# Optimization experiments

Hardware: AMD Instinct MI355X
Metric: run time of the kernel (lower is better)

Reference implementation:

```python
import jax, jax.numpy as jnp
import numpy as np

B, D, H, W = 4, 64, 64, 64
S = 64          # number of attention segments
N = 8192        # query pixels
K = 4           # n_refs
HID = 256
D9 = D * 9      # feat_unfold 3x3
IN_DIM = D9 + 2 + 2  # +rel_coord +rel_cell


def setup_inputs() -> dict:
    key = jax.random.key(0)
    ks = jax.random.split(key, 10)
    feat = jax.random.normal(ks[0], (B, D, H, W), jnp.float32)
    attn_sftmx = jax.nn.softmax(jax.random.normal(ks[1], (B, H * W, S), jnp.float32), axis=2)
    coord = jax.random.uniform(ks[2], (B, N, 2), jnp.float32) * 2.0 - 1.0  # [-1,1]
    cell = jnp.full((B, N, 2), 2.0 / 256.0, jnp.float32)  # HR cell size for 256x256 output
    def lin(k, fi, fo):
        return jax.random.normal(k, (fi, fo), jnp.float32) / np.sqrt(fi).astype(np.float32)
    w0 = lin(ks[3], IN_DIM, HID); b0 = jnp.zeros((HID,), jnp.float32)
    w1 = lin(ks[4], HID, HID);    b1 = jnp.zeros((HID,), jnp.float32)
    w2 = lin(ks[5], HID, HID);    b2 = jnp.zeros((HID,), jnp.float32)
    w3 = lin(ks[6], HID, HID);    b3 = jnp.zeros((HID,), jnp.float32)
    w4 = lin(ks[7], HID, 3);      b4 = jnp.zeros((3,), jnp.float32)
    return dict(feat=feat, attn_sftmx=attn_sftmx, coord=coord, cell=cell,
                w0=w0, b0=b0, w1=w1, b1=b1, w2=w2, b2=b2, w3=w3, b3=b3, w4=w4, b4=b4)


def _imnet(x, w0, b0, w1, b1, w2, b2, w3, b3, w4, b4):
    h = jax.nn.relu(x @ w0 + b0)
    h = jax.nn.relu(h @ w1 + b1)
    h = jax.nn.relu(h @ w2 + b2)
    h = jax.nn.relu(h @ w3 + b3)
    return h @ w4 + b4


def reference(feat, attn_sftmx, coord, cell, w0, b0, w1, b1, w2, b2, w3, b3, w4, b4):
    Bn, Dc, h, w = feat.shape
    Nq = coord.shape[1]
    hw = h * w
    # ---- feat_unfold: F.unfold(feat, 3, padding=1) -> (B, D*9, h, w), channel order c*9 + ki*3 + kj
    pad = jnp.pad(feat, ((0, 0), (0, 0), (1, 1), (1, 1)))
    patches = jnp.stack([pad[:, :, ki:ki + h, kj:kj + w]
                         for ki in range(3) for kj in range(3)], axis=2)  # (B,D,9,h,w)
    d9 = Dc * 9
    feat_rows = patches.reshape(Bn, d9, h, w).transpose(0, 2, 3, 1).reshape(Bn, hw, d9)  # (B,hw,D9)
    scale_hw = jnp.array([h, w], jnp.float32)
    rel_cell = cell * scale_hw  # (B,N,2)

    # ================= attention ensemble =================
    pc = (coord + 1.0) / 2.0 * scale_hw
    pc = jnp.clip(pc.astype(jnp.int32), 0, hw - 1)
    pc1d = pc[..., 0] * h + pc[..., 1]  # (B,N)
    segm_idx_whole = jnp.argmax(attn_sftmx, axis=2)  # (B,hw)
    segm_idx = jnp.take_along_axis(segm_idx_whole, pc1d, axis=1)  # (B,N)
    attn_t = attn_sftmx.transpose(0, 2, 1)  # (B,S,hw)
    prob_map = jnp.take_along_axis(attn_t, segm_idx[:, :, None], axis=1)  # (B,N,hw)
    ref_probs, ref_coords = jax.lax.top_k(prob_map, K)  # (B,N,K)
    # Faithful to original: ref_coords (values in [0,hw)) index the FLATTENED (B*hw, D9)
    # feature table, i.e. all batches gather batch-0 rows (source-code behavior).
    ref_feats = feat_rows.reshape(Bn * hw, d9)[ref_coords]  # (B,N,K,D9)
    rrc = ref_coords - pc1d[..., None]  # (B,N,K) int
    rel0 = jnp.floor_divide(rrc, h).astype(jnp.float32) / h
    rel1 = jnp.mod(rrc, h).astype(jnp.float32) / w
    rel = jnp.stack([rel0, rel1], axis=-1)  # (B,N,K,2)
    rc_b = jnp.broadcast_to(rel_cell[:, :, None, :], (Bn, Nq, K, 2))
    inp_attn = jnp.concatenate([ref_feats, rel, rc_b], axis=-1)  # (B,N,K,IN)
    pred_attn = _imnet(inp_attn.reshape(-1, inp_attn.shape[-1]),
                       w0, b0, w1, b1, w2, b2, w3, b3, w4, b4).reshape(Bn, Nq, K, -1)
    wprob = ref_probs / jnp.sum(ref_probs, axis=-1, keepdims=True)
    ret_attn = jnp.sum(pred_attn * wprob[..., None], axis=2)  # (B,N,3)

    # ================= local ensemble =================
    rx, ry = 1.0 / h, 1.0 / w  # 2/h/2, 2/w/2
    eps = 1e-6
    offs = jnp.array([[-1., -1.], [-1., 1.], [1., -1.], [1., 1.]], jnp.float32) \
           * jnp.array([rx, ry], jnp.float32) + eps  # (4,2)
    c = jnp.clip(coord[None] + offs[:, None, None, :], -1 + 1e-6, 1 - 1e-6)  # (4,B,N,2)
    # grid_sample nearest, align_corners=False (grid flipped -> c[...,0] is height)
    iy = jnp.clip(jnp.rint(((c[..., 0] + 1.0) * h - 1.0) / 2.0), 0, h - 1).astype(jnp.int32)
    ix = jnp.clip(jnp.rint(((c[..., 1] + 1.0) * w - 1.0) / 2.0), 0, w - 1).astype(jnp.int32)
    flat = iy * w + ix  # (4,B,N)
    bidx = jnp.arange(Bn)[None, :, None]
    q_feat = feat_rows[bidx, flat]  # (4,B,N,D9)
    qc0 = -1.0 + (2.0 * iy.astype(jnp.float32) + 1.0) / h  # make_coord centers
    qc1 = -1.0 + (2.0 * ix.astype(jnp.float32) + 1.0) / w
    rel_coord = jnp.stack([(coord[None, ..., 0] - qc0) * h,
                           (coord[None, ..., 1] - qc1) * w], axis=-1)  # (4,B,N,2)
    rc_l = jnp.broadcast_to(rel_cell[None], (4, Bn, Nq, 2))
    inp_loc = jnp.concatenate([q_feat, rel_coord, rc_l], axis=-1)  # (4,B,N,IN)
    pred_loc = _imnet(inp_loc.reshape(-1, inp_loc.shape[-1]),
                      w0, b0, w1, b1, w2, b2, w3, b3, w4, b4).reshape(4, Bn, Nq, -1)
    area = jnp.abs(rel_coord[..., 0] * rel_coord[..., 1]) + 1e-9  # (4,B,N)
    tot = jnp.sum(area, axis=0)
    wts = area[::-1] / tot[None]  # area swap 0<->3, 1<->2 == reverse
    ret_local = jnp.sum(pred_loc * wts[..., None], axis=0)  # (B,N,3)

    total = float(K + 4)
    return ret_attn * (K / total) + ret_local * (4.0 / total)
```

## Files before the change

### kernel.cpp

```cpp
#include <hip/hip_runtime.h>
#include <hip/hip_bf16.h>
#include <math.h>
#include <stdint.h>

#define B_ 4
#define D_ 64
#define H_ 64
#define W_ 64
#define S_ 64
#define N_ 8192
#define K_ 4
#define HID_ 256
#define HW_ 4096
#define NQ_ (B_*N_)
#define ROWS_ (NQ_*8)

typedef _Float16 h8   __attribute__((ext_vector_type(8)));
typedef _Float16 h4   __attribute__((ext_vector_type(4)));
typedef float    f32x4 __attribute__((ext_vector_type(4)));

__global__ void fused_prep_kernel(const float* __restrict__ feat,
                                  const float* __restrict__ attn,
                                  const float* __restrict__ w0,
                                  const float* __restrict__ w1,
                                  const float* __restrict__ w2,
                                  const float* __restrict__ w3,
                                  const float* __restrict__ w4,
                                  _Float16* __restrict__ featT,
                                  float* __restrict__ attnT,
                                  _Float16* __restrict__ w0F,
                                  _Float16* __restrict__ wF123,
                                  float* __restrict__ w4T,
                                  float* __restrict__ w0tail,
                                  int* __restrict__ segm)
{
  __shared__ float t[64][65];
  int blk = blockIdx.x;
  int tid = threadIdx.x;

  if (blk < 256) {
    int b = blk >> 6, y = blk & 63;
    for (int p = 0; p < 16; ++p) {
      int c = p * 4 + (tid >> 6), x = tid & 63;
      t[c][x] = feat[(((size_t)b * 64 + c) << 12) + (y << 6) + x];
    }
    __syncthreads();
    for (int p = 0; p < 16; ++p) {
      int x = p * 4 + (tid >> 6), c = tid & 63;
      featT[((((size_t)b * 64 + y) * 64 + x) << 6) + c] = (_Float16)t[c][x];
    }
    return;
  }
  blk -= 256;
  if (blk < 256) {
    int b = blk >> 6, j0 = (blk & 63) << 6;
    for (int idx = tid; idx < 4096; idx += 256) {
      int r = idx >> 6, c = idx & 63;
      t[r][c] = attn[((size_t)(b * 4096 + j0 + r)) * 64 + c];
    }
    __syncthreads();
    for (int idx = tid; idx < 4096; idx += 256) {
      int s = idx >> 6, r = idx & 63;
      attnT[((size_t)(b * 64 + s)) * 4096 + j0 + r] = t[r][s];
    }
    return;
  }
  blk -= 256;
  if (blk < 1351) {
    int i = blk * 256 + tid;
    if (i < 147456) {
      int g = i / 36864, rem = i - g * 36864;
      int ks = rem >> 11, rem2 = rem & 2047;
      int cb = rem2 >> 9, e = rem2 & 511;
      int lane = e >> 3, j = e & 7;
      int n = g * 64 + cb * 16 + (lane & 15);
      int k = ks * 32 + (lane >> 4) * 8 + j;
      int kk = k >> 6, cc = k & 63;
      w0F[i] = (_Float16)w0[(cc * 9 + kk) * 256 + n];
      return;
    }
    i -= 147456;
    if (i < 196608) {
      int l = i >> 16, rem = i & 65535;
      int g = rem >> 14, rem2 = rem & 16383;
      int ks = rem2 >> 11, rem3 = rem2 & 2047;
      int cb = rem3 >> 9, e = rem3 & 511;
      int lane = e >> 3, j = e & 7;
      int n = g * 64 + cb * 16 + (lane & 15);
      int k = ks * 32 + (lane >> 4) * 8 + j;
      const float* w = (l == 0) ? w1 : (l == 1) ? w2 : w3;
      wF123[i] = (_Float16)w[k * 256 + n];
      return;
    }
    i -= 196608;
    if (i < 768) { int j = i / 256, c = i - j * 256; w4T[i] = w4[c * 3 + j]; return; }
    i -= 768;
    if (i < 1024) { int j = i >> 8, n = i & 255; w0tail[i] = w0[(576 + j) * 256 + n]; }
    return;
  }
  blk -= 1351;
  {
    int p = blk * 256 + tid;
    if (p >= B_ * HW_) return;
    const float* a = attn + (size_t)p * S_;
    float best = a[0]; int bi = 0;
    for (int s = 1; s < S_; ++s) { float v = a[s]; if (v > best) { best = v; bi = s; } }
    segm[p] = bi;
  }
}

__global__ void topk_kernel(const float* __restrict__ attnT,
                            int* __restrict__ refc, float* __restrict__ wprob)
{
  int bid = blockIdx.x;
  int tid = threadIdx.x;
  __shared__ float sv[256]; __shared__ int si[256];
  __shared__ float cvs[4]; __shared__ int cis[4];

  const float* col = attnT + (size_t)bid * 4096;
  float tv[4] = { -INFINITY, -INFINITY, -INFINITY, -INFINITY };
  int   ti[4] = { 0x7fffffff, 0x7fffffff, 0x7fffffff, 0x7fffffff };
  for (int j = tid; j < HW_; j += 256) {
    float v = col[j];
    if (v > tv[3]) {
      tv[3] = v; ti[3] = j;
      #pragma unroll
      for (int x = 3; x > 0; --x) {
        if (tv[x] > tv[x-1] || (tv[x] == tv[x-1] && ti[x] < ti[x-1])) {
          float fv = tv[x]; tv[x] = tv[x-1]; tv[x-1] = fv;
          int   fi = ti[x]; ti[x] = ti[x-1]; ti[x-1] = fi;
        }
      }
    }
  }
  int ptr = 0;
  for (int r = 0; r < 4; ++r) {
    sv[tid] = (ptr < 4) ? tv[ptr] : -INFINITY;
    si[tid] = (ptr < 4) ? ti[ptr] : 0x7fffffff;
    __syncthreads();
    for (int o = 128; o; o >>= 1) {
      if (tid < o) {
        float v2 = sv[tid + o]; int i2 = si[tid + o];
        if (v2 > sv[tid] || (v2 == sv[tid] && i2 < si[tid])) { sv[tid] = v2; si[tid] = i2; }
      }
      __syncthreads();
    }
    if (tid == 0) { cvs[r] = sv[0]; cis[r] = si[0]; }
    __syncthreads();
    if (ptr < 4 && ti[ptr] == cis[r]) ptr++;
    __syncthreads();
  }
  if (tid == 0) {
    float ssum = cvs[0] + cvs[1] + cvs[2] + cvs[3];
    for (int k = 0; k < 4; ++k) { refc[bid*4 + k] = cis[k]; wprob[bid*4 + k] = cvs[k] / ssum; }
  }
}

__global__ void meta_kernel(const float* __restrict__ coord, const float* __restrict__ cell,
                            const int* __restrict__ segm, const int* __restrict__ refc,
                            const float* __restrict__ wprob,
                            int* __restrict__ msrc, float4* __restrict__ mt,
                            float* __restrict__ mwgt)
{
  int q = blockIdx.x * 256 + threadIdx.x;
  if (q >= NQ_) return;
  int b = q >> 13;
  float c0 = coord[2*q], c1 = coord[2*q + 1];
  float rc0 = cell[2*q] * 64.0f, rc1 = cell[2*q + 1] * 64.0f;

  float pf0 = (c0 + 1.0f) / 2.0f * 64.0f;
  float pf1 = (c1 + 1.0f) / 2.0f * 64.0f;
  int pc0 = (int)pf0, pc1 = (int)pf1;
  pc0 = min(max(pc0, 0), 4095); pc1 = min(max(pc1, 0), 4095);
  int pc1d = pc0 * 64 + pc1;
  int sg = segm[b * 4096 + min(pc1d, 4095)];
  int base = (b * 64 + sg) * 4;
  #pragma unroll
  for (int k = 0; k < 4; ++k) {
    int rc = refc[base + k];
    int rrc = rc - pc1d;
    float rel0 = (float)(rrc >> 6) * 0.015625f;
    float rel1 = (float)(rrc & 63) * 0.015625f;
    int r = q * 8 + k;
    msrc[r] = rc;
    mt[r] = make_float4(rel0, rel1, rc0, rc1);
    mwgt[r] = 0.5f * wprob[base + k];
  }

  const float sg0[4] = { -1.f, -1.f, 1.f, 1.f };
  const float sg1[4] = { -1.f,  1.f, -1.f, 1.f };
  float area[4], rr0[4], rr1[4]; int srcs[4];
  #pragma unroll
  for (int t = 0; t < 4; ++t) {
    float o0 = sg0[t] * 0.015625f + 1e-6f;
    float o1 = sg1[t] * 0.015625f + 1e-6f;
    float cc0 = fminf(fmaxf(c0 + o0, -1.0f + 1e-6f), 1.0f - 1e-6f);
    float cc1 = fminf(fmaxf(c1 + o1, -1.0f + 1e-6f), 1.0f - 1e-6f);
    float vy = ((cc0 + 1.0f) * 64.0f - 1.0f) / 2.0f;
    float vx = ((cc1 + 1.0f) * 64.0f - 1.0f) / 2.0f;
    float fy = fminf(fmaxf(rintf(vy), 0.0f), 63.0f);
    float fx = fminf(fmaxf(rintf(vx), 0.0f), 63.0f);
    int iy = (int)fy, ix = (int)fx;
    srcs[t] = b * 4096 + iy * 64 + ix;
    float qc0 = -1.0f + (2.0f * (float)iy + 1.0f) / 64.0f;
    float qc1 = -1.0f + (2.0f * (float)ix + 1.0f) / 64.0f;
    float r0 = (c0 - qc0) * 64.0f;
    float r1 = (c1 - qc1) * 64.0f;
    rr0[t] = r0; rr1[t] = r1;
    area[t] = fabsf(r0 * r1) + 1e-9f;
  }
  float tot = area[0] + area[1] + area[2] + area[3];
  #pragma unroll
  for (int t = 0; t < 4; ++t) {
    int r = q * 8 + 4 + t;
    msrc[r] = srcs[t];
    mt[r] = make_float4(rr0[t], rr1[t], rc0, rc1);
    mwgt[r] = 0.5f * area[3 - t] / tot;
  }
}

__launch_bounds__(256, 4)
__global__ void p0_kernel(const _Float16* __restrict__ featT,
                          const _Float16* __restrict__ w0F,
                          float* __restrict__ P0)
{
  int blk = blockIdx.x;
  int b = blk >> 8, y = (blk >> 2) & 63, qr = blk & 3;
  int tid = threadIdx.x;
  int wave = tid >> 6, lane = tid & 63, quad = lane >> 4, l16 = lane & 15;

  f32x4 acc[4];
  #pragma unroll
  for (int j = 0; j < 4; j++) { f32x4 z = {0.f,0.f,0.f,0.f}; acc[j] = z; }
  h8 zero8 = {0,0,0,0,0,0,0,0};

  #pragma unroll
  for (int ks = 0; ks < 18; ++ks) {
    int k0 = ks * 32 + quad * 8;
    int kk = k0 >> 6, cc = k0 & 63;
    int di = kk / 3 - 1, dj = kk - (kk / 3) * 3 - 1;
    int yy = y + di;
    int xx = qr * 16 + l16 + dj;
    h8 afr;
    if ((unsigned)yy < 64u && (unsigned)xx < 64u)
      afr = *(const h8*)(featT + ((((size_t)b * 64 + yy) * 64 + xx) << 6) + cc);
    else
      afr = zero8;
    #pragma unroll
    for (int cb = 0; cb < 4; cb++) {
      h8 bfr = *(const h8*)(w0F + ((((size_t)wave * 18 + ks) * 4 + cb) << 9) + lane * 8);
      acc[cb] = __builtin_amdgcn_mfma_f32_16x16x32_f16(afr, bfr, acc[cb], 0, 0, 0);
    }
  }
  int pixbase = (b * 4096 + y * 64 + qr * 16);
  #pragma unroll
  for (int cb = 0; cb < 4; cb++)
    #pragma unroll
    for (int i = 0; i < 4; i++) {
      int m = quad * 4 + i;
      int n = wave * 64 + cb * 16 + l16;
      P0[((size_t)(pixbase + m) << 8) + n] = acc[cb][i];
    }
}

__launch_bounds__(256, 2)
__global__ void trunk_kernel(const float* __restrict__ P0,
                             const int* __restrict__ msrc,
                             const float4* __restrict__ mt,
                             const float* __restrict__ mwgt,
                             const float* __restrict__ w0tail,
                             const float* __restrict__ b0,
                             const _Float16* __restrict__ wF123,
                             const float* __restrict__ b1,
                             const float* __restrict__ b2,
                             const float* __restrict__ b3,
                             const float* __restrict__ w4T,
                             const float* __restrict__ b4,
                             float* __restrict__ out)
{
  __shared__ _Float16 hS[128][264];
  __shared__ float part_s[128][2][3];
  __shared__ float red[128][4];

  int tid = threadIdx.x;
  int rowbase = blockIdx.x * 128;
  int wv = tid >> 6;

  {
    int cg = tid & 63;
    float4 wt0 = ((const float4*)w0tail)[cg];
    float4 wt1 = ((const float4*)w0tail)[64 + cg];
    float4 wt2 = ((const float4*)w0tail)[128 + cg];
    float4 wt3 = ((const float4*)w0tail)[192 + cg];
    float4 bb  = ((const float4*)b0)[cg];
    #pragma unroll 1
    for (int g = 0; g < 4; ++g) {
      int srcs[8]; float4 ts[8];
      #pragma unroll
      for (int i = 0; i < 8; ++i) {
        int r = rowbase + g * 32 + i * 4 + wv;
        srcs[i] = msrc[r];
        ts[i] = mt[r];
      }
      #pragma unroll
      for (int i = 0; i < 8; ++i) {
        int rr = g * 32 + i * 4 + wv;
        float4 t = ts[i];
        float4 p = ((const float4*)(P0 + ((size_t)srcs[i] << 8)))[cg];
        h4 v;
        v[0] = (_Float16)fmaxf(p.x + t.x*wt0.x + t.y*wt1.x + t.z*wt2.x + t.w*wt3.x + bb.x, 0.0f);
        v[1] = (_Float16)fmaxf(p.y + t.x*wt0.y + t.y*wt1.y + t.z*wt2.y + t.w*wt3.y + bb.y, 0.0f);
        v[2] = (_Float16)fmaxf(p.z + t.x*wt0.z + t.y*wt1.z + t.z*wt2.z + t.w*wt3.z + bb.z, 0.0f);
        v[3] = (_Float16)fmaxf(p.w + t.x*wt0.w + t.y*wt1.w + t.z*wt2.w + t.w*wt3.w + bb.w, 0.0f);
        *(h4*)(&hS[rr][cg * 4]) = v;
      }
    }
  }
  __syncthreads();

  int wave = tid >> 6, lane = tid & 63, quad = lane >> 4, l16 = lane & 15;

  #pragma unroll 1
  for (int l = 0; l < 3; ++l) {
    const _Float16* wL = wF123 + (((size_t)l * 4 + wave) << 14);
    const float* bia = (l == 0) ? b1 : (l == 1) ? b2 : b3;
    f32x4 acc[8][4];
    #pragma unroll
    for (int i = 0; i < 8; i++)
      #pragma unroll
      for (int j = 0; j < 4; j++) { f32x4 z = {0.f,0.f,0.f,0.f}; acc[i][j] = z; }

    h8 bP[2][4];
    #pragma unroll
    for (int cb = 0; cb < 4; cb++) {
      bP[0][cb] = *(const h8*)(wL + (((size_t)0 * 4 + cb) << 9) + lane * 8);
      bP[1][cb] = *(const h8*)(wL + (((size_t)1 * 4 + cb) << 9) + lane * 8);
    }

    #pragma unroll
    for (int ks = 0; ks < 8; ++ks) {
      int cur = ks & 1;
      int k0 = ks * 32 + quad * 8;
      h8 afr[8];
      #pragma unroll
      for (int rb = 0; rb < 8; rb++)
        afr[rb] = *(const h8*)(&hS[rb * 16 + l16][k0]);
      #pragma unroll
      for (int rb = 0; rb < 8; rb++)
        #pragma unroll
        for (int cb = 0; cb < 4; cb++)
          acc[rb][cb] = __builtin_amdgcn_mfma_f32_16x16x32_f16(afr[rb], bP[cur][cb], acc[rb][cb], 0, 0, 0);
      if (ks + 2 < 8) {
        #pragma unroll
        for (int cb = 0; cb < 4; cb++)
          bP[cur][cb] = *(const h8*)(wL + (((size_t)(ks + 2) * 4 + cb) << 9) + lane * 8);
      }
    }
    __syncthreads();
    #pragma unroll
    for (int rb = 0; rb < 8; rb++)
      #pragma unroll
      for (int cb = 0; cb < 4; cb++) {
        int n = wave * 64 + cb * 16 + l16;
        float bv = bia[n];
        #pragma unroll
        for (int i = 0; i < 4; i++) {
          int m = rb * 16 + quad * 4 + i;
          hS[m][n] = (_Float16)fmaxf(acc[rb][cb][i] + bv, 0.0f);
        }
      }
    __syncthreads();
  }

  {
    int row = tid >> 1, part = tid & 1;
    const _Float16* hr = &hS[row][part * 128];
    float s0 = 0.f, s1 = 0.f, s2 = 0.f;
    #pragma unroll
    for (int c8 = 0; c8 < 128; c8 += 8) {
      h8 hv = *(const h8*)(hr + c8);
      #pragma unroll
      for (int u = 0; u < 8; ++u) {
        float h = (float)hv[u];
        int c = part * 128 + c8 + u;
        s0 += h * w4T[c];
        s1 += h * w4T[256 + c];
        s2 += h * w4T[512 + c];
      }
    }
    part_s[row][part][0] = s0; part_s[row][part][1] = s1; part_s[row][part][2] = s2;
  }
  __syncthreads();
  if (tid < 128) {
    float wgt = mwgt[rowbase + tid];
    red[tid][0] = (part_s[tid][0][0] + part_s[tid][1][0] + b4[0]) * wgt;
    red[tid][1] = (part_s[tid][0][1] + part_s[tid][1][1] + b4[1]) * wgt;
    red[tid][2] = (part_s[tid][0][2] + part_s[tid][1][2] + b4[2]) * wgt;
  }
  __syncthreads();
  if (tid < 16) {
    int q = blockIdx.x * 16 + tid;
    float o0 = 0.f, o1 = 0.f, o2 = 0.f;
    #pragma unroll
    for (int j = 0; j < 8; j++) {
      o0 += red[tid * 8 + j][0];
      o1 += red[tid * 8 + j][1];
      o2 += red[tid * 8 + j][2];
    }
    out[q * 3 + 0] = o0;
    out[q * 3 + 1] = o1;
    out[q * 3 + 2] = o2;
  }
}

extern "C" void kernel_launch(void* const* d_in, const int* in_sizes, int n_in,
                              void* d_out, int out_size, void* d_ws, size_t ws_size,
                              hipStream_t stream)
{
  const float* feat  = (const float*)d_in[0];
  const float* attn  = (const float*)d_in[1];
  const float* coord = (const float*)d_in[2];
  const float* cell  = (const float*)d_in[3];
  const float* w0 = (const float*)d_in[4];
  const float* b0 = (const float*)d_in[5];
  const float* w1 = (const float*)d_in[6];
  const float* b1 = (const float*)d_in[7];
  const float* w2 = (const float*)d_in[8];
  const float* b2 = (const float*)d_in[9];
  const float* w3 = (const float*)d_in[10];
  const float* b3 = (const float*)d_in[11];
  const float* w4 = (const float*)d_in[12];
  const float* b4 = (const float*)d_in[13];
  float* out = (float*)d_out;

  char* ws = (char*)d_ws;
  size_t off = 0;
  auto alloc = [&](size_t bytes) -> char* {
    char* p = ws + off;
    off += (bytes + 255) & ~(size_t)255;
    return p;
  };
  _Float16* featT = (_Float16*)alloc((size_t)B_ * H_ * W_ * D_ * 2);
  _Float16* w0F   = (_Float16*)alloc((size_t)147456 * 2);
  _Float16* wF123 = (_Float16*)alloc((size_t)196608 * 2);
  float*  w4T   = (float*)alloc((size_t)3 * 256 * 4);
  float*  w0tl  = (float*)alloc((size_t)4 * 256 * 4);
  float*  attnT = (float*)alloc((size_t)B_ * S_ * HW_ * 4);
  int*    segm  = (int*)alloc((size_t)B_ * HW_ * 4);
  int*    refc  = (int*)alloc((size_t)B_ * S_ * K_ * 4);
  float*  wprob = (float*)alloc((size_t)B_ * S_ * K_ * 4);
  float*  P0    = (float*)alloc((size_t)B_ * HW_ * 256 * 4);
  int*    msrc  = (int*)alloc((size_t)ROWS_ * 4);
  float4* mtb   = (float4*)alloc((size_t)ROWS_ * 16);
  float*  mwgt  = (float*)alloc((size_t)ROWS_ * 4);
  (void)in_sizes; (void)n_in; (void)out_size; (void)ws_size;

  fused_prep_kernel<<<1927, 256, 0, stream>>>(feat, attn, w0, w1, w2, w3, w4,
                                              featT, attnT, w0F, wF123, w4T, w0tl, segm);
  topk_kernel<<<256, 256, 0, stream>>>(attnT, refc, wprob);
  meta_kernel<<<128, 256, 0, stream>>>(coord, cell, segm, refc, wprob, msrc, mtb, mwgt);
  p0_kernel<<<1024, 256, 0, stream>>>(featT, w0F, P0);
  trunk_kernel<<<2048, 256, 0, stream>>>(P0, msrc, mtb, mwgt, w0tl, b0, wF123,
                                         b1, b2, b3, w4T, b4, out);
}
```

Baseline: 302.2 us.

## Store P0 in fp16, widen p0 tiles, and reorder final linear reduction

The p0 kernel now computes a full 64-pixel row per block with 4x4 MFMA accumulators, so each block loads the weight fragments once instead of once per 16-pixel quarter. P0 is written as fp16 instead of fp32, which halves both the write traffic and the gathered reads in the trunk. The final layer now takes the weighted sum over each query's 8 rows before the 256x3 dot product, using linearity, and scales b4 by the summed weights. This cuts the last-layer multiply work by about 8x. The cost is lower occupancy in p0, fewer blocks in its grid, and extra fp16 rounding of the precomputed first-layer activations.

```diff
diff --git a/kernel.cpp b/kernel.cpp
--- a/kernel.cpp
+++ b/kernel.cpp
@@ -219,19 +219,21 @@
   }
 }
 
-__launch_bounds__(256, 4)
+__launch_bounds__(256, 2)
 __global__ void p0_kernel(const _Float16* __restrict__ featT,
                           const _Float16* __restrict__ w0F,
-                          float* __restrict__ P0)
+                          _Float16* __restrict__ P0h)
 {
   int blk = blockIdx.x;
-  int b = blk >> 8, y = (blk >> 2) & 63, qr = blk & 3;
+  int b = blk >> 6, y = blk & 63;
   int tid = threadIdx.x;
   int wave = tid >> 6, lane = tid & 63, quad = lane >> 4, l16 = lane & 15;
 
-  f32x4 acc[4];
-  #pragma unroll
-  for (int j = 0; j < 4; j++) { f32x4 z = {0.f,0.f,0.f,0.f}; acc[j] = z; }
+  f32x4 acc[4][4];
+  #pragma unroll
+  for (int i = 0; i < 4; i++)
+    #pragma unroll
+    for (int j = 0; j < 4; j++) { f32x4 z = {0.f,0.f,0.f,0.f}; acc[i][j] = z; }
   h8 zero8 = {0,0,0,0,0,0,0,0};
 
   #pragma unroll
@@ -240,31 +242,40 @@
     int kk = k0 >> 6, cc = k0 & 63;
     int di = kk / 3 - 1, dj = kk - (kk / 3) * 3 - 1;
     int yy = y + di;
-    int xx = qr * 16 + l16 + dj;
-    h8 afr;
-    if ((unsigned)yy < 64u && (unsigned)xx < 64u)
-      afr = *(const h8*)(featT + ((((size_t)b * 64 + yy) * 64 + xx) << 6) + cc);
-    else
-      afr = zero8;
-    #pragma unroll
-    for (int cb = 0; cb < 4; cb++) {
-      h8 bfr = *(const h8*)(w0F + ((((size_t)wave * 18 + ks) * 4 + cb) << 9) + lane * 8);
-      acc[cb] = __builtin_amdgcn_mfma_f32_16x16x32_f16(afr, bfr, acc[cb], 0, 0, 0);
-    }
-  }
-  int pixbase = (b * 4096 + y * 64 + qr * 16);
-  #pragma unroll
-  for (int cb = 0; cb < 4; cb++)
-    #pragma unroll
-    for (int i = 0; i < 4; i++) {
-      int m = quad * 4 + i;
-      int n = wave * 64 + cb * 16 + l16;
-      P0[((size_t)(pixbase + m) << 8) + n] = acc[cb][i];
-    }
+    h8 afr[4];
+    #pragma unroll
+    for (int rb = 0; rb < 4; rb++) {
+      int xx = rb * 16 + l16 + dj;
+      if ((unsigned)yy < 64u && (unsigned)xx < 64u)
+        afr[rb] = *(const h8*)(featT + ((((size_t)b * 64 + yy) * 64 + xx) << 6) + cc);
+      else
+        afr[rb] = zero8;
+    }
+    h8 bfr[4];
+    #pragma unroll
+    for (int cb = 0; cb < 4; cb++)
+      bfr[cb] = *(const h8*)(w0F + ((((size_t)wave * 18 + ks) * 4 + cb) << 9) + lane * 8);
+    #pragma unroll
+    for (int rb = 0; rb < 4; rb++)
+      #pragma unroll
+      for (int cb = 0; cb < 4; cb++)
+        acc[rb][cb] = __builtin_amdgcn_mfma_f32_16x16x32_f16(afr[rb], bfr[cb], acc[rb][cb], 0, 0, 0);
+  }
+  int pixbase = blk * 64;
+  #pragma unroll
+  for (int rb = 0; rb < 4; rb++)
+    #pragma unroll
+    for (int cb = 0; cb < 4; cb++)
+      #pragma unroll
+      for (int i = 0; i < 4; i++) {
+        int m = rb * 16 + quad * 4 + i;
+        int n = wave * 64 + cb * 16 + l16;
+        P0h[((size_t)(pixbase + m) << 8) + n] = (_Float16)acc[rb][cb][i];
+      }
 }
 
 __launch_bounds__(256, 2)
-__global__ void trunk_kernel(const float* __restrict__ P0,
+__global__ void trunk_kernel(const _Float16* __restrict__ P0h,
                              const int* __restrict__ msrc,
                              const float4* __restrict__ mt,
                              const float* __restrict__ mwgt,
@@ -279,12 +290,15 @@
                              float* __restrict__ out)
 {
   __shared__ _Float16 hS[128][264];
-  __shared__ float part_s[128][2][3];
-  __shared__ float red[128][4];
+  __shared__ float mwL[128];
+  __shared__ float swL[16];
+  __shared__ float partB[16][3][4];
 
   int tid = threadIdx.x;
   int rowbase = blockIdx.x * 128;
   int wv = tid >> 6;
+
+  if (tid < 128) mwL[tid] = mwgt[rowbase + tid];
 
   {
     int cg = tid & 63;
@@ -306,12 +320,12 @@
       for (int i = 0; i < 8; ++i) {
         int rr = g * 32 + i * 4 + wv;
         float4 t = ts[i];
-        float4 p = ((const float4*)(P0 + ((size_t)srcs[i] << 8)))[cg];
+        h4 pv = *(const h4*)(P0h + ((size_t)srcs[i] << 8) + cg * 4);
         h4 v;
-        v[0] = (_Float16)fmaxf(p.x + t.x*wt0.x + t.y*wt1.x + t.z*wt2.x + t.w*wt3.x + bb.x, 0.0f);
-        v[1] = (_Float16)fmaxf(p.y + t.x*wt0.y + t.y*wt1.y + t.z*wt2.y + t.w*wt3.y + bb.y, 0.0f);
-        v[2] = (_Float16)fmaxf(p.z + t.x*wt0.z + t.y*wt1.z + t.z*wt2.z + t.w*wt3.z + bb.z, 0.0f);
-        v[3] = (_Float16)fmaxf(p.w + t.x*wt0.w + t.y*wt1.w + t.z*wt2.w + t.w*wt3.w + bb.w, 0.0f);
+        v[0] = (_Float16)fmaxf((float)pv[0] + t.x*wt0.x + t.y*wt1.x + t.z*wt2.x + t.w*wt3.x + bb.x, 0.0f);
+        v[1] = (_Float16)fmaxf((float)pv[1] + t.x*wt0.y + t.y*wt1.y + t.z*wt2.y + t.w*wt3.y + bb.y, 0.0f);
+        v[2] = (_Float16)fmaxf((float)pv[2] + t.x*wt0.z + t.y*wt1.z + t.z*wt2.z + t.w*wt3.z + bb.z, 0.0f);
+        v[3] = (_Float16)fmaxf((float)pv[3] + t.x*wt0.w + t.y*wt1.w + t.z*wt2.w + t.w*wt3.w + bb.w, 0.0f);
         *(h4*)(&hS[rr][cg * 4]) = v;
       }
     }
@@ -373,43 +387,49 @@
   }
 
   {
-    int row = tid >> 1, part = tid & 1;
-    const _Float16* hr = &hS[row][part * 128];
-    float s0 = 0.f, s1 = 0.f, s2 = 0.f;
-    #pragma unroll
-    for (int c8 = 0; c8 < 128; c8 += 8) {
-      h8 hv = *(const h8*)(hr + c8);
+    int q = tid >> 4, cpart = tid & 15;
+    float accq[16];
+    #pragma unroll
+    for (int u = 0; u < 16; ++u) accq[u] = 0.0f;
+    float sw = 0.0f;
+    #pragma unroll
+    for (int j = 0; j < 8; ++j) {
+      int row = q * 8 + j;
+      float w = mwL[row];
+      sw += w;
+      h8 a = *(const h8*)(&hS[row][cpart * 16]);
+      h8 bq = *(const h8*)(&hS[row][cpart * 16 + 8]);
       #pragma unroll
       for (int u = 0; u < 8; ++u) {
-        float h = (float)hv[u];
-        int c = part * 128 + c8 + u;
-        s0 += h * w4T[c];
-        s1 += h * w4T[256 + c];
-        s2 += h * w4T[512 + c];
-      }
-    }
-    part_s[row][part][0] = s0; part_s[row][part][1] = s1; part_s[row][part][2] = s2;
+        accq[u]     += w * (float)a[u];
+        accq[8 + u] += w * (float)bq[u];
+      }
+    }
+    __syncthreads();
+    float* hsF = (float*)&hS[0][0];
+    #pragma unroll
+    for (int u = 0; u < 16; u += 4)
+      *(f32x4*)(hsF + q * 256 + cpart * 16 + u) =
+        f32x4{accq[u], accq[u+1], accq[u+2], accq[u+3]};
+    if (cpart == 0) swL[q] = sw;
   }
   __syncthreads();
-  if (tid < 128) {
-    float wgt = mwgt[rowbase + tid];
-    red[tid][0] = (part_s[tid][0][0] + part_s[tid][1][0] + b4[0]) * wgt;
-    red[tid][1] = (part_s[tid][0][1] + part_s[tid][1][1] + b4[1]) * wgt;
-    red[tid][2] = (part_s[tid][0][2] + part_s[tid][1][2] + b4[2]) * wgt;
+  if (tid < 192) {
+    int q = tid / 12, r = tid % 12, j = r >> 2, part = r & 3;
+    const float* hsF = (const float*)&hS[0][0];
+    const float* hp = hsF + q * 256 + part * 64;
+    const float* wp = w4T + j * 256 + part * 64;
+    float s = 0.0f;
+    #pragma unroll
+    for (int u = 0; u < 64; ++u) s += hp[u] * wp[u];
+    partB[q][j][part] = s;
   }
   __syncthreads();
-  if (tid < 16) {
-    int q = blockIdx.x * 16 + tid;
-    float o0 = 0.f, o1 = 0.f, o2 = 0.f;
-    #pragma unroll
-    for (int j = 0; j < 8; j++) {
-      o0 += red[tid * 8 + j][0];
-      o1 += red[tid * 8 + j][1];
-      o2 += red[tid * 8 + j][2];
-    }
-    out[q * 3 + 0] = o0;
-    out[q * 3 + 1] = o1;
-    out[q * 3 + 2] = o2;
+  if (tid < 48) {
+    int q = tid / 3, j = tid % 3;
+    float o = partB[q][j][0] + partB[q][j][1] + partB[q][j][2] + partB[q][j][3]
+            + b4[j] * swL[q];
+    out[(size_t)(blockIdx.x * 16 + q) * 3 + j] = o;
   }
 }
 
@@ -449,7 +469,7 @@
   int*    segm  = (int*)alloc((size_t)B_ * HW_ * 4);
   int*    refc  = (int*)alloc((size_t)B_ * S_ * K_ * 4);
   float*  wprob = (float*)alloc((size_t)B_ * S_ * K_ * 4);
-  float*  P0    = (float*)alloc((size_t)B_ * HW_ * 256 * 4);
+  _Float16* P0h = (_Float16*)alloc((size_t)B_ * HW_ * 256 * 2);
   int*    msrc  = (int*)alloc((size_t)ROWS_ * 4);
   float4* mtb   = (float4*)alloc((size_t)ROWS_ * 16);
   float*  mwgt  = (float*)alloc((size_t)ROWS_ * 4);
@@ -459,7 +479,7 @@
                                               featT, attnT, w0F, wF123, w4T, w0tl, segm);
   topk_kernel<<<256, 256, 0, stream>>>(attnT, refc, wprob);
   meta_kernel<<<128, 256, 0, stream>>>(coord, cell, segm, refc, wprob, msrc, mtb, mwgt);
-  p0_kernel<<<1024, 256, 0, stream>>>(featT, w0F, P0);
-  trunk_kernel<<<2048, 256, 0, stream>>>(P0, msrc, mtb, mwgt, w0tl, b0, wF123,
+  p0_kernel<<<256, 256, 0, stream>>>(featT, w0F, P0h);
+  trunk_kernel<<<2048, 256, 0, stream>>>(P0h, msrc, mtb, mwgt, w0tl, b0, wF123,
                                          b1, b2, b3, w4T, b4, out);
 }
```

Result: faster. 270.5 us (-10.5%).
